# Optimization experiments

Measured on AMD Instinct MI355X. Metric: run time of the kernel, lower is better.

Reference implementation:

```python
import jax, jax.numpy as jnp
import numpy as np

EPS = 1e-12
ALPHA = 0.2  # LeakyReLU negative slope
N_NODES = 100000
N_EDGES = 1600000
F = 128
H = 8

def setup_inputs() -> dict:
    key = jax.random.key(0)
    k1, k2, k3, k4 = jax.random.split(key, 4)
    x = jax.random.normal(k1, (N_NODES, F), dtype=jnp.float32)
    row = jax.random.randint(k2, (N_EDGES,), 0, N_NODES, dtype=jnp.int32)
    col = jax.random.randint(k3, (N_EDGES,), 0, N_NODES, dtype=jnp.int32)
    # xavier_uniform with gain=1.414 on [H, 2F]
    limit = 1.414 * np.sqrt(6.0 / (H + 2 * F))
    aa = jax.random.uniform(k4, (H, 2 * F), dtype=jnp.float32, minval=-limit, maxval=limit)
    return {"x": x, "row": row, "col": col, "aa": aa}

def reference(x, row, col, aa):
    # e = leakyrelu(aa @ cat(x[row], x[col], dim=1).T)  -> [H, E]
    # Split aa so per-node scores are computed once, then gathered per edge
    # (identical math, avoids materializing the [E, 2F] concat).
    a_src, a_dst = aa[:, :F], aa[:, F:]          # [H, F] each
    s_src = x @ a_src.T                           # [N, H]
    s_dst = x @ a_dst.T                           # [N, H]
    e = s_src[row] + s_dst[col]                   # [E, H]
    e = jnp.where(e > 0, e, ALPHA * e)            # LeakyReLU
    # scatter_softmax over edges grouped by row (per head)
    m = jax.ops.segment_max(e, row, num_segments=N_NODES)  # [N, H]
    m = jnp.where(jnp.isfinite(m), m, 0.0)        # empty segments -> -inf; neutralize
    ex = jnp.exp(e - m[row])                      # [E, H]
    s = jax.ops.segment_sum(ex, row, num_segments=N_NODES)  # [N, H]
    a = ex / (s[row] + EPS)                       # [E, H]
    return a.T                                    # [H, E] to match torch layout
```

## Files before the change

kernel.cpp:

```cpp
#include <hip/hip_runtime.h>

constexpr int N_NODES = 100000;
constexpr int N_EDGES = 1600000;
constexpr int F = 128;
constexpr int H = 8;
constexpr float ALPHA = 0.2f;
constexpr float EPSF = 1e-12f;

constexpr int PSHIFT = 8;
constexpr int PN = 1 << PSHIFT;
constexpr int NPART = (N_NODES + PN - 1) / PN;
constexpr int MAXPART = 5120;
constexpr int EPB = 4096;
constexpr int OCAP = 4096;

constexpr int KA_BLOCKS = (N_EDGES + EPB - 1) / EPB;
constexpr int K1_BLOCKS = (N_NODES + 1023) / 1024;

static_assert(N_EDGES % 64 == 0, "k4_hs assumes 64-edge blocks");

__global__ void __launch_bounds__(1024)
kA1_fused(const int* __restrict__ row, const int* __restrict__ col,
          int* __restrict__ gcnt, unsigned* __restrict__ part,
          int* __restrict__ ocnt, int2* __restrict__ olist,
          const float* __restrict__ x, const float* __restrict__ aa,
          float* __restrict__ srn, float* __restrict__ sd) {
    __shared__ int hist[NPART];
    __shared__ int base[NPART];
    __shared__ float sa[H * 2 * F];
    const int t = threadIdx.x;

    if (blockIdx.x < KA_BLOCKS) {
        const int e0 = blockIdx.x * EPB;
        constexpr int K = EPB / 1024;
        int rr[K], cc[K];
        for (int p = t; p < NPART; p += 1024) hist[p] = 0;
        __syncthreads();
#pragma unroll
        for (int k = 0; k < K; ++k) {
            int i = e0 + k * 1024 + t;
            if (i < N_EDGES) {
                rr[k] = row[i];
                cc[k] = col[i];
                atomicAdd(&hist[rr[k] >> PSHIFT], 1);
            } else rr[k] = -1;
        }
        __syncthreads();
        for (int p = t; p < NPART; p += 1024) {
            int h = hist[p];
            base[p] = h ? atomicAdd(&gcnt[p], h) : 0;
            hist[p] = 0;
        }
        __syncthreads();
#pragma unroll
        for (int k = 0; k < K; ++k) {
            if (rr[k] >= 0) {
                int r = rr[k], c = cc[k];
                int p = r >> PSHIFT;
                int slot = base[p] + atomicAdd(&hist[p], 1);
                unsigned pk = ((unsigned)(r & (PN - 1)) << 17) | (unsigned)c;
                if (slot < MAXPART) {
                    part[(size_t)p * MAXPART + slot] = pk;
                } else {
                    int q = atomicAdd(ocnt, 1);
                    if (q < OCAP) olist[q] = make_int2(p, (int)pk);
                }
            }
        }
    } else {
        if (t < 512) reinterpret_cast<float4*>(sa)[t] =
            reinterpret_cast<const float4*>(aa)[t];
        __syncthreads();
        int node = (blockIdx.x - KA_BLOCKS) * 1024 + t;
        if (node >= N_NODES) return;
        const float4* xr = reinterpret_cast<const float4*>(x + (size_t)node * F);
        float accs[H], accd[H];
#pragma unroll
        for (int h = 0; h < H; ++h) { accs[h] = 0.f; accd[h] = 0.f; }
        for (int f4 = 0; f4 < F / 4; ++f4) {
            float4 xv = xr[f4];
#pragma unroll
            for (int h = 0; h < H; ++h) {
                float4 av = *reinterpret_cast<const float4*>(&sa[h * 2 * F + 4 * f4]);
                float4 bv = *reinterpret_cast<const float4*>(&sa[h * 2 * F + F + 4 * f4]);
                accs[h] += xv.x * av.x + xv.y * av.y + xv.z * av.z + xv.w * av.w;
                accd[h] += xv.x * bv.x + xv.y * bv.y + xv.z * bv.z + xv.w * bv.w;
            }
        }
        float4* os = reinterpret_cast<float4*>(srn + (size_t)node * 16);
        os[0] = make_float4(accs[0], accs[1], accs[2], accs[3]);
        os[1] = make_float4(accs[4], accs[5], accs[6], accs[7]);
        float4* od = reinterpret_cast<float4*>(sd + (size_t)node * H);
        od[0] = make_float4(accd[0], accd[1], accd[2], accd[3]);
        od[1] = make_float4(accd[4], accd[5], accd[6], accd[7]);
    }
}

__global__ void __launch_bounds__(1024)
kB_sum(const float* __restrict__ sd, const unsigned* __restrict__ part,
       const int* __restrict__ gcnt, const int* __restrict__ ocnt,
       const int2* __restrict__ olist, float* __restrict__ srn) {
    __shared__ unsigned plist[MAXPART];
    __shared__ unsigned sorted_c[MAXPART];
    __shared__ int hist[PN];
    __shared__ int off[PN + 1];
    __shared__ int cur[PN];
    __shared__ float ssrc[PN * H];
    const int p = blockIdx.x;
    const int t = threadIdx.x;
    const int nbase = p << PSHIFT;

    for (int i = t; i < PN; i += 1024) hist[i] = 0;
    for (int j = t; j < PN * H; j += 1024) {
        int n = nbase + (j >> 3);
        ssrc[j] = (n < N_NODES) ? srn[(size_t)n * 16 + (j & 7)] : 0.f;
    }
    __syncthreads();

    int cnt = gcnt[p]; if (cnt > MAXPART) cnt = MAXPART;
    const unsigned* pp = part + (size_t)p * MAXPART;

    for (int i = t; i < cnt; i += 1024) {
        unsigned pk = pp[i];
        plist[i] = pk;
        atomicAdd(&hist[pk >> 17], 1);
    }
    __syncthreads();

    if (t < 64) {
        int h0 = hist[4 * t], h1 = hist[4 * t + 1];
        int h2 = hist[4 * t + 2], h3 = hist[4 * t + 3];
        int s0 = h0, s1 = s0 + h1, s2 = s1 + h2, s3 = s2 + h3;
        int sc = s3;
#pragma unroll
        for (int d = 1; d < 64; d <<= 1) {
            int v = __shfl_up(sc, d);
            if (t >= d) sc += v;
        }
        int prefix = sc - s3;
        off[4 * t + 1] = prefix + s0; off[4 * t + 2] = prefix + s1;
        off[4 * t + 3] = prefix + s2; off[4 * t + 4] = prefix + s3;
        cur[4 * t]     = prefix;      cur[4 * t + 1] = prefix + s0;
        cur[4 * t + 2] = prefix + s1; cur[4 * t + 3] = prefix + s2;
        if (t == 0) off[0] = 0;
    }
    __syncthreads();

    for (int i = t; i < cnt; i += 1024) {
        unsigned pk = plist[i];
        int rl = (int)(pk >> 17);
        int slot = atomicAdd(&cur[rl], 1);
        sorted_c[slot] = pk & 0x1FFFFu;
    }
    __syncthreads();

    int mo = *ocnt; if (mo > OCAP) mo = OCAP;
    {
        int nl = t >> 2, pi = t & 3;
        int node = nbase + nl;
        int k0 = off[nl], k1e = off[nl + 1];
        float s0 = ssrc[nl * 8 + 2 * pi];
        float s1 = ssrc[nl * 8 + 2 * pi + 1];
        float a0 = 0.f, a1 = 0.f;
        int k = k0;
        for (; k + 4 <= k1e; k += 4) {
            int c0 = (int)sorted_c[k],     c1 = (int)sorted_c[k + 1];
            int c2 = (int)sorted_c[k + 2], c3 = (int)sorted_c[k + 3];
            float2 d0 = *reinterpret_cast<const float2*>(&sd[(size_t)c0 * H + 2 * pi]);
            float2 d1 = *reinterpret_cast<const float2*>(&sd[(size_t)c1 * H + 2 * pi]);
            float2 d2 = *reinterpret_cast<const float2*>(&sd[(size_t)c2 * H + 2 * pi]);
            float2 d3 = *reinterpret_cast<const float2*>(&sd[(size_t)c3 * H + 2 * pi]);
            float e;
            e = s0 + d0.x; e = e > 0.f ? e : ALPHA * e; a0 += __expf(e);
            e = s1 + d0.y; e = e > 0.f ? e : ALPHA * e; a1 += __expf(e);
            e = s0 + d1.x; e = e > 0.f ? e : ALPHA * e; a0 += __expf(e);
            e = s1 + d1.y; e = e > 0.f ? e : ALPHA * e; a1 += __expf(e);
            e = s0 + d2.x; e = e > 0.f ? e : ALPHA * e; a0 += __expf(e);
            e = s1 + d2.y; e = e > 0.f ? e : ALPHA * e; a1 += __expf(e);
            e = s0 + d3.x; e = e > 0.f ? e : ALPHA * e; a0 += __expf(e);
            e = s1 + d3.y; e = e > 0.f ? e : ALPHA * e; a1 += __expf(e);
        }
        for (; k < k1e; ++k) {
            int c = (int)sorted_c[k];
            float2 d = *reinterpret_cast<const float2*>(&sd[(size_t)c * H + 2 * pi]);
            float e0 = s0 + d.x; e0 = e0 > 0.f ? e0 : ALPHA * e0;
            float e1 = s1 + d.y; e1 = e1 > 0.f ? e1 : ALPHA * e1;
            a0 += __expf(e0); a1 += __expf(e1);
        }
        for (int j = 0; j < mo; ++j) {
            int2 oe = olist[j];
            if (oe.x == p && (int)(((unsigned)oe.y) >> 17) == nl) {
                int c = oe.y & 0x1FFFF;
                float2 d = *reinterpret_cast<const float2*>(&sd[(size_t)c * H + 2 * pi]);
                float e0 = s0 + d.x; e0 = e0 > 0.f ? e0 : ALPHA * e0;
                float e1 = s1 + d.y; e1 = e1 > 0.f ? e1 : ALPHA * e1;
                a0 += __expf(e0); a1 += __expf(e1);
            }
        }
        if (node < N_NODES) {
            srn[(size_t)node * 16 + 8 + 2 * pi]     = 1.f / (a0 + EPSF);
            srn[(size_t)node * 16 + 8 + 2 * pi + 1] = 1.f / (a1 + EPSF);
        }
    }
}

__global__ void __launch_bounds__(512)
k4_hs(const int* __restrict__ row, const int* __restrict__ col,
      const float* __restrict__ srn, const float* __restrict__ sd,
      float* __restrict__ out) {
    __shared__ int ridx[64], cidx[64];
    __shared__ float sm[8][72];
    const int e0 = blockIdx.x * 64;
    const int t = threadIdx.x;
    if (t < 64) ridx[t] = row[e0 + t];
    else if (t < 128) cidx[t - 64] = col[e0 + t - 64];
    __syncthreads();
    {
        int el = t >> 3, h = t & 7;
        int r = ridx[el], c = cidx[el];
        float s  = srn[(size_t)r * 16 + h];
        float rv = srn[(size_t)r * 16 + 8 + h];
        float d  = sd[(size_t)c * H + h];
        float e = s + d;
        e = e > 0.f ? e : ALPHA * e;
        sm[h][el] = __expf(e) * rv;
    }
    __syncthreads();
    {
        int h2 = t >> 6, j = t & 63;
        out[(size_t)h2 * N_EDGES + e0 + j] = sm[h2][j];
    }
}

__global__ void k1_scores(const float* __restrict__ x, const float* __restrict__ aa,
                          float* __restrict__ srn, float* __restrict__ sd) {
    __shared__ float sa[H * 2 * F];
    for (int i = threadIdx.x; i < H * 2 * F; i += blockDim.x) sa[i] = aa[i];
    __syncthreads();
    int node = blockIdx.x * blockDim.x + threadIdx.x;
    if (node >= N_NODES) return;
    const float4* xr = reinterpret_cast<const float4*>(x + (size_t)node * F);
    float accs[H], accd[H];
#pragma unroll
    for (int h = 0; h < H; ++h) { accs[h] = 0.f; accd[h] = 0.f; }
    for (int f4 = 0; f4 < F / 4; ++f4) {
        float4 xv = xr[f4];
#pragma unroll
        for (int h = 0; h < H; ++h) {
            float4 av = *reinterpret_cast<const float4*>(&sa[h * 2 * F + 4 * f4]);
            float4 bv = *reinterpret_cast<const float4*>(&sa[h * 2 * F + F + 4 * f4]);
            accs[h] += xv.x * av.x + xv.y * av.y + xv.z * av.z + xv.w * av.w;
            accd[h] += xv.x * bv.x + xv.y * bv.y + xv.z * bv.z + xv.w * bv.w;
        }
    }
    float4* os = reinterpret_cast<float4*>(srn + (size_t)node * 16);
    os[0] = make_float4(accs[0], accs[1], accs[2], accs[3]);
    os[1] = make_float4(accs[4], accs[5], accs[6], accs[7]);
    float4* od = reinterpret_cast<float4*>(sd + (size_t)node * H);
    od[0] = make_float4(accd[0], accd[1], accd[2], accd[3]);
    od[1] = make_float4(accd[4], accd[5], accd[6], accd[7]);
}

__global__ void kz_zero_sums(float* __restrict__ srn) {
    int t = blockIdx.x * blockDim.x + threadIdx.x;
    if (t >= N_NODES * H) return;
    srn[(size_t)(t >> 3) * 16 + 8 + (t & 7)] = 0.f;
}

__global__ void k3nm_sum(const float* __restrict__ srn_ro, const float* __restrict__ s_dst,
                         const int* __restrict__ row, const int* __restrict__ col,
                         float* __restrict__ srn) {
    int i = blockIdx.x * blockDim.x + threadIdx.x;
    if (i >= N_EDGES) return;
    int r = row[i], c = col[i];
    const float4* sr = reinterpret_cast<const float4*>(srn_ro + (size_t)r * 16);
    float4 a0 = sr[0], a1 = sr[1];
    const float4* sc = reinterpret_cast<const float4*>(s_dst + (size_t)c * H);
    float4 b0 = sc[0], b1 = sc[1];
    float ev[H] = {a0.x + b0.x, a0.y + b0.y, a0.z + b0.z, a0.w + b0.w,
                   a1.x + b1.x, a1.y + b1.y, a1.z + b1.z, a1.w + b1.w};
#pragma unroll
    for (int h = 0; h < H; ++h) {
        float e = ev[h] > 0.f ? ev[h] : ALPHA * ev[h];
        atomicAdd(&srn[(size_t)r * 16 + 8 + h], __expf(e));
    }
}

__global__ void k_inv(float* __restrict__ srn) {
    int t = blockIdx.x * blockDim.x + threadIdx.x;
    if (t >= N_NODES * H) return;
    int n = t >> 3, h = t & 7;
    float s = srn[(size_t)n * 16 + 8 + h];
    srn[(size_t)n * 16 + 8 + h] = 1.0f / (s + EPSF);
}

__global__ void k4_out(const int* __restrict__ row, const int* __restrict__ col,
                       const float* __restrict__ srn, const float* __restrict__ s_dst,
                       float* __restrict__ out) {
    int i = blockIdx.x * blockDim.x + threadIdx.x;
    if (i >= N_EDGES) return;
    int r = row[i], c = col[i];
    const float4* sr = reinterpret_cast<const float4*>(srn + (size_t)r * 16);
    float4 a0 = sr[0], a1 = sr[1], r0 = sr[2], r1 = sr[3];
    const float4* sc = reinterpret_cast<const float4*>(s_dst + (size_t)c * H);
    float4 b0 = sc[0], b1 = sc[1];
    float ev[H] = {a0.x + b0.x, a0.y + b0.y, a0.z + b0.z, a0.w + b0.w,
                   a1.x + b1.x, a1.y + b1.y, a1.z + b1.z, a1.w + b1.w};
    float rv[H] = {r0.x, r0.y, r0.z, r0.w, r1.x, r1.y, r1.z, r1.w};
#pragma unroll
    for (int h = 0; h < H; ++h) {
        float e = ev[h] > 0.f ? ev[h] : ALPHA * ev[h];
        out[(size_t)h * N_EDGES + i] = __expf(e) * rv[h];
    }
}

extern "C" void kernel_launch(void* const* d_in, const int* in_sizes, int n_in,
                              void* d_out, int out_size, void* d_ws, size_t ws_size,
                              hipStream_t stream) {
    const float* x   = (const float*)d_in[0];
    const int*   row = (const int*)d_in[1];
    const int*   col = (const int*)d_in[2];
    const float* aa  = (const float*)d_in[3];
    float* out = (float*)d_out;

    float*    srn  = (float*)d_ws;
    float*    sd   = srn + (size_t)N_NODES * 16;
    unsigned* part = (unsigned*)(sd + (size_t)N_NODES * H);
    int*      gcnt = (int*)(part + (size_t)NPART * MAXPART);
    int*      ocnt = gcnt + NPART;
    int2*     olist = (int2*)(ocnt + 16);

    const size_t need_b = ((size_t)N_NODES * 24 + (size_t)NPART * MAXPART
                           + NPART + 16 + 2 * OCAP) * 4;

    const int B = 256;
    const int GE = (N_EDGES + B - 1) / B;
    const int GN = (N_NODES + B - 1) / B;

    if (ws_size >= need_b) {
        hipMemsetAsync(gcnt, 0, (size_t)(NPART + 16) * sizeof(int), stream);
        kA1_fused<<<KA_BLOCKS + K1_BLOCKS, 1024, 0, stream>>>(
            row, col, gcnt, part, ocnt, olist, x, aa, srn, sd);
        kB_sum<<<NPART, 1024, 0, stream>>>(sd, part, gcnt, ocnt, olist, srn);
        k4_hs<<<N_EDGES / 64, 512, 0, stream>>>(row, col, srn, sd, out);
    } else {
        k1_scores<<<GN, B, 0, stream>>>(x, aa, srn, sd);
        kz_zero_sums<<<(N_NODES * H + B - 1) / B, B, 0, stream>>>(srn);
        k3nm_sum<<<GE, B, 0, stream>>>(srn, sd, row, col, srn);
        k_inv<<<(N_NODES * H + B - 1) / B, B, 0, stream>>>(srn);
        k4_out<<<GE, B, 0, stream>>>(row, col, srn, sd, out);
    }
}
```

Before: 211.2 us.

## Replace global-atomic partition bucketing with per-block fixed-capacity cells

The edge bucketing pass stops using global atomics and a memset. Each 256-thread block now writes its edges into fixed 24-slot cells per partition, plus a small per-block overflow list. The sum kernel gathers the cells for its partition from all producer blocks, building its histogram and counting sort straight from global memory. The score blocks also compute two nodes per thread with smaller blocks. In exchange, the cell array is sparse and strided to read, the sum kernel reads the part buffer twice, and overflow handling walks every block's overflow list.

```diff
diff --git a/kernel.cpp b/kernel.cpp
--- a/kernel.cpp
+++ b/kernel.cpp
@@ -10,120 +10,139 @@
 constexpr int PSHIFT = 8;
 constexpr int PN = 1 << PSHIFT;
 constexpr int NPART = (N_NODES + PN - 1) / PN;
-constexpr int MAXPART = 5120;
 constexpr int EPB = 4096;
-constexpr int OCAP = 4096;
-
 constexpr int KA_BLOCKS = (N_EDGES + EPB - 1) / EPB;
-constexpr int K1_BLOCKS = (N_NODES + 1023) / 1024;
+constexpr int CAP = 24;
+constexpr int OC2 = 32;
+constexpr int K1_NPB = 512;
+constexpr int K1_BLOCKS = (N_NODES + K1_NPB - 1) / K1_NPB;
+constexpr int NCELL = NPART * CAP;
 
 static_assert(N_EDGES % 64 == 0, "k4_hs assumes 64-edge blocks");
 
-__global__ void __launch_bounds__(1024)
+__global__ void __launch_bounds__(256)
 kA1_fused(const int* __restrict__ row, const int* __restrict__ col,
-          int* __restrict__ gcnt, unsigned* __restrict__ part,
-          int* __restrict__ ocnt, int2* __restrict__ olist,
+          unsigned* __restrict__ part2, int* __restrict__ cnt2,
+          int* __restrict__ ocnt2, int2* __restrict__ oflow2,
           const float* __restrict__ x, const float* __restrict__ aa,
           float* __restrict__ srn, float* __restrict__ sd) {
-    __shared__ int hist[NPART];
-    __shared__ int base[NPART];
-    __shared__ float sa[H * 2 * F];
     const int t = threadIdx.x;
-
     if (blockIdx.x < KA_BLOCKS) {
-        const int e0 = blockIdx.x * EPB;
-        constexpr int K = EPB / 1024;
-        int rr[K], cc[K];
-        for (int p = t; p < NPART; p += 1024) hist[p] = 0;
+        __shared__ int lcnt[NPART];
+        __shared__ int lof;
+        const int b = blockIdx.x;
+        const int e0 = b * EPB;
+        for (int p = t; p < NPART; p += 256) lcnt[p] = 0;
+        if (t == 0) lof = 0;
         __syncthreads();
 #pragma unroll
-        for (int k = 0; k < K; ++k) {
-            int i = e0 + k * 1024 + t;
+        for (int k = 0; k < EPB / 256; ++k) {
+            int i = e0 + k * 256 + t;
             if (i < N_EDGES) {
-                rr[k] = row[i];
-                cc[k] = col[i];
-                atomicAdd(&hist[rr[k] >> PSHIFT], 1);
-            } else rr[k] = -1;
-        }
-        __syncthreads();
-        for (int p = t; p < NPART; p += 1024) {
-            int h = hist[p];
-            base[p] = h ? atomicAdd(&gcnt[p], h) : 0;
-            hist[p] = 0;
-        }
-        __syncthreads();
-#pragma unroll
-        for (int k = 0; k < K; ++k) {
-            if (rr[k] >= 0) {
-                int r = rr[k], c = cc[k];
+                int r = row[i], c = col[i];
                 int p = r >> PSHIFT;
-                int slot = base[p] + atomicAdd(&hist[p], 1);
                 unsigned pk = ((unsigned)(r & (PN - 1)) << 17) | (unsigned)c;
-                if (slot < MAXPART) {
-                    part[(size_t)p * MAXPART + slot] = pk;
+                int slot = atomicAdd(&lcnt[p], 1);
+                if (slot < CAP) {
+                    part2[((size_t)p * KA_BLOCKS + b) * CAP + slot] = pk;
                 } else {
-                    int q = atomicAdd(ocnt, 1);
-                    if (q < OCAP) olist[q] = make_int2(p, (int)pk);
+                    int q = atomicAdd(&lof, 1);
+                    if (q < OC2) oflow2[b * OC2 + q] = make_int2(p, (int)pk);
                 }
             }
         }
+        __syncthreads();
+        for (int p = t; p < NPART; p += 256) {
+            int v = lcnt[p];
+            cnt2[(size_t)b * NPART + p] = v < CAP ? v : CAP;
+        }
+        if (t == 0) { int v = lof; ocnt2[b] = v < OC2 ? v : OC2; }
     } else {
-        if (t < 512) reinterpret_cast<float4*>(sa)[t] =
-            reinterpret_cast<const float4*>(aa)[t];
+        __shared__ float sa[H * 2 * F];
+        reinterpret_cast<float4*>(sa)[t]       = reinterpret_cast<const float4*>(aa)[t];
+        reinterpret_cast<float4*>(sa)[t + 256] = reinterpret_cast<const float4*>(aa)[t + 256];
         __syncthreads();
-        int node = (blockIdx.x - KA_BLOCKS) * 1024 + t;
-        if (node >= N_NODES) return;
-        const float4* xr = reinterpret_cast<const float4*>(x + (size_t)node * F);
-        float accs[H], accd[H];
-#pragma unroll
-        for (int h = 0; h < H; ++h) { accs[h] = 0.f; accd[h] = 0.f; }
+        const int q = blockIdx.x - KA_BLOCKS;
+        int n0 = q * K1_NPB + t;
+        int n1 = n0 + 256;
+        int n0c = n0 < N_NODES ? n0 : N_NODES - 1;
+        int n1c = n1 < N_NODES ? n1 : N_NODES - 1;
+        const float4* xr0 = reinterpret_cast<const float4*>(x + (size_t)n0c * F);
+        const float4* xr1 = reinterpret_cast<const float4*>(x + (size_t)n1c * F);
+        float a0s[H], a0d[H], a1s[H], a1d[H];
+#pragma unroll
+        for (int h = 0; h < H; ++h) { a0s[h] = 0.f; a0d[h] = 0.f; a1s[h] = 0.f; a1d[h] = 0.f; }
         for (int f4 = 0; f4 < F / 4; ++f4) {
-            float4 xv = xr[f4];
+            float4 xv0 = xr0[f4];
+            float4 xv1 = xr1[f4];
 #pragma unroll
             for (int h = 0; h < H; ++h) {
                 float4 av = *reinterpret_cast<const float4*>(&sa[h * 2 * F + 4 * f4]);
                 float4 bv = *reinterpret_cast<const float4*>(&sa[h * 2 * F + F + 4 * f4]);
-                accs[h] += xv.x * av.x + xv.y * av.y + xv.z * av.z + xv.w * av.w;
-                accd[h] += xv.x * bv.x + xv.y * bv.y + xv.z * bv.z + xv.w * bv.w;
+                a0s[h] += xv0.x * av.x + xv0.y * av.y + xv0.z * av.z + xv0.w * av.w;
+                a0d[h] += xv0.x * bv.x + xv0.y * bv.y + xv0.z * bv.z + xv0.w * bv.w;
+                a1s[h] += xv1.x * av.x + xv1.y * av.y + xv1.z * av.z + xv1.w * av.w;
+                a1d[h] += xv1.x * bv.x + xv1.y * bv.y + xv1.z * bv.z + xv1.w * bv.w;
             }
         }
-        float4* os = reinterpret_cast<float4*>(srn + (size_t)node * 16);
-        os[0] = make_float4(accs[0], accs[1], accs[2], accs[3]);
-        os[1] = make_float4(accs[4], accs[5], accs[6], accs[7]);
-        float4* od = reinterpret_cast<float4*>(sd + (size_t)node * H);
-        od[0] = make_float4(accd[0], accd[1], accd[2], accd[3]);
-        od[1] = make_float4(accd[4], accd[5], accd[6], accd[7]);
+        if (n0 < N_NODES) {
+            float4* os = reinterpret_cast<float4*>(srn + (size_t)n0 * 16);
+            os[0] = make_float4(a0s[0], a0s[1], a0s[2], a0s[3]);
+            os[1] = make_float4(a0s[4], a0s[5], a0s[6], a0s[7]);
+            float4* od = reinterpret_cast<float4*>(sd + (size_t)n0 * H);
+            od[0] = make_float4(a0d[0], a0d[1], a0d[2], a0d[3]);
+            od[1] = make_float4(a0d[4], a0d[5], a0d[6], a0d[7]);
+        }
+        if (n1 < N_NODES) {
+            float4* os = reinterpret_cast<float4*>(srn + (size_t)n1 * 16);
+            os[0] = make_float4(a1s[0], a1s[1], a1s[2], a1s[3]);
+            os[1] = make_float4(a1s[4], a1s[5], a1s[6], a1s[7]);
+            float4* od = reinterpret_cast<float4*>(sd + (size_t)n1 * H);
+            od[0] = make_float4(a1d[0], a1d[1], a1d[2], a1d[3]);
+            od[1] = make_float4(a1d[4], a1d[5], a1d[6], a1d[7]);
+        }
     }
 }
 
 __global__ void __launch_bounds__(1024)
-kB_sum(const float* __restrict__ sd, const unsigned* __restrict__ part,
-       const int* __restrict__ gcnt, const int* __restrict__ ocnt,
-       const int2* __restrict__ olist, float* __restrict__ srn) {
-    __shared__ unsigned plist[MAXPART];
-    __shared__ unsigned sorted_c[MAXPART];
+kB_sum(const float* __restrict__ sd, const unsigned* __restrict__ part2,
+       const int* __restrict__ cnt2, const int* __restrict__ ocnt2,
+       const int2* __restrict__ oflow2, float* __restrict__ srn) {
+    __shared__ unsigned sorted_c[NCELL];
     __shared__ int hist[PN];
     __shared__ int off[PN + 1];
     __shared__ int cur[PN];
     __shared__ float ssrc[PN * H];
+    __shared__ int lcb[NPART];
+    __shared__ int locnt[NPART];
+    __shared__ int otot;
     const int p = blockIdx.x;
     const int t = threadIdx.x;
     const int nbase = p << PSHIFT;
 
+    if (t == 0) otot = 0;
     for (int i = t; i < PN; i += 1024) hist[i] = 0;
     for (int j = t; j < PN * H; j += 1024) {
         int n = nbase + (j >> 3);
         ssrc[j] = (n < N_NODES) ? srn[(size_t)n * 16 + (j & 7)] : 0.f;
     }
-    __syncthreads();
-
-    int cnt = gcnt[p]; if (cnt > MAXPART) cnt = MAXPART;
-    const unsigned* pp = part + (size_t)p * MAXPART;
-
-    for (int i = t; i < cnt; i += 1024) {
-        unsigned pk = pp[i];
-        plist[i] = pk;
-        atomicAdd(&hist[pk >> 17], 1);
+    for (int b = t; b < NPART; b += 1024) {
+        lcb[b] = cnt2[(size_t)b * NPART + p];
+        int v = ocnt2[b];
+        locnt[b] = v;
+        if (v) atomicAdd(&otot, v);
+    }
+    __syncthreads();
+
+    const unsigned* pbase = part2 + (size_t)p * KA_BLOCKS * CAP;
+
+    for (int j = t; j < NCELL; j += 1024) {
+        int b = (int)(((unsigned)j * 21846u) >> 19);
+        int s = j - b * CAP;
+        if (s < lcb[b]) {
+            unsigned pk = pbase[(size_t)b * CAP + s];
+            atomicAdd(&hist[pk >> 17], 1);
+        }
     }
     __syncthreads();
 
@@ -146,15 +165,17 @@
     }
     __syncthreads();
 
-    for (int i = t; i < cnt; i += 1024) {
-        unsigned pk = plist[i];
-        int rl = (int)(pk >> 17);
-        int slot = atomicAdd(&cur[rl], 1);
-        sorted_c[slot] = pk & 0x1FFFFu;
-    }
-    __syncthreads();
-
-    int mo = *ocnt; if (mo > OCAP) mo = OCAP;
+    for (int j = t; j < NCELL; j += 1024) {
+        int b = (int)(((unsigned)j * 21846u) >> 19);
+        int s = j - b * CAP;
+        if (s < lcb[b]) {
+            unsigned pk = pbase[(size_t)b * CAP + s];
+            int slot = atomicAdd(&cur[pk >> 17], 1);
+            sorted_c[slot] = pk & 0x1FFFFu;
+        }
+    }
+    __syncthreads();
+
     {
         int nl = t >> 2, pi = t & 3;
         int node = nbase + nl;
@@ -187,14 +208,19 @@
             float e1 = s1 + d.y; e1 = e1 > 0.f ? e1 : ALPHA * e1;
             a0 += __expf(e0); a1 += __expf(e1);
         }
-        for (int j = 0; j < mo; ++j) {
-            int2 oe = olist[j];
-            if (oe.x == p && (int)(((unsigned)oe.y) >> 17) == nl) {
-                int c = oe.y & 0x1FFFF;
-                float2 d = *reinterpret_cast<const float2*>(&sd[(size_t)c * H + 2 * pi]);
-                float e0 = s0 + d.x; e0 = e0 > 0.f ? e0 : ALPHA * e0;
-                float e1 = s1 + d.y; e1 = e1 > 0.f ? e1 : ALPHA * e1;
-                a0 += __expf(e0); a1 += __expf(e1);
+        if (otot > 0) {
+            for (int b = 0; b < NPART; ++b) {
+                int m = locnt[b];
+                for (int j = 0; j < m; ++j) {
+                    int2 e2 = oflow2[b * OC2 + j];
+                    if (e2.x == p && (int)(((unsigned)e2.y) >> 17) == nl) {
+                        int c = e2.y & 0x1FFFF;
+                        float2 d = *reinterpret_cast<const float2*>(&sd[(size_t)c * H + 2 * pi]);
+                        float e0 = s0 + d.x; e0 = e0 > 0.f ? e0 : ALPHA * e0;
+                        float e1 = s1 + d.y; e1 = e1 > 0.f ? e1 : ALPHA * e1;
+                        a0 += __expf(e0); a1 += __expf(e1);
+                    }
+                }
             }
         }
         if (node < N_NODES) {
@@ -323,27 +349,30 @@
     const float* aa  = (const float*)d_in[3];
     float* out = (float*)d_out;
 
-    float*    srn  = (float*)d_ws;
-    float*    sd   = srn + (size_t)N_NODES * 16;
-    unsigned* part = (unsigned*)(sd + (size_t)N_NODES * H);
-    int*      gcnt = (int*)(part + (size_t)NPART * MAXPART);
-    int*      ocnt = gcnt + NPART;
-    int2*     olist = (int2*)(ocnt + 16);
-
-    const size_t need_b = ((size_t)N_NODES * 24 + (size_t)NPART * MAXPART
-                           + NPART + 16 + 2 * OCAP) * 4;
+    float*    srn   = (float*)d_ws;
+    float*    sd    = srn + (size_t)N_NODES * 16;
+    unsigned* part2 = (unsigned*)(sd + (size_t)N_NODES * H);
+    int*      cnt2  = (int*)(part2 + (size_t)NPART * KA_BLOCKS * CAP);
+    int*      ocnt2 = cnt2 + (size_t)KA_BLOCKS * NPART;
+    int2*     oflow2 = (int2*)(ocnt2 + KA_BLOCKS);
+
+    const size_t need_full = (size_t)(N_NODES * 24) * 4
+                           + (size_t)NPART * KA_BLOCKS * CAP * 4
+                           + (size_t)KA_BLOCKS * NPART * 4
+                           + (size_t)KA_BLOCKS * 4
+                           + (size_t)KA_BLOCKS * OC2 * 8;
+    const size_t need_min  = (size_t)N_NODES * (16 + 8) * 4;
 
     const int B = 256;
     const int GE = (N_EDGES + B - 1) / B;
     const int GN = (N_NODES + B - 1) / B;
 
-    if (ws_size >= need_b) {
-        hipMemsetAsync(gcnt, 0, (size_t)(NPART + 16) * sizeof(int), stream);
-        kA1_fused<<<KA_BLOCKS + K1_BLOCKS, 1024, 0, stream>>>(
-            row, col, gcnt, part, ocnt, olist, x, aa, srn, sd);
-        kB_sum<<<NPART, 1024, 0, stream>>>(sd, part, gcnt, ocnt, olist, srn);
+    if (ws_size >= need_full) {
+        kA1_fused<<<KA_BLOCKS + K1_BLOCKS, 256, 0, stream>>>(
+            row, col, part2, cnt2, ocnt2, oflow2, x, aa, srn, sd);
+        kB_sum<<<NPART, 1024, 0, stream>>>(sd, part2, cnt2, ocnt2, oflow2, srn);
         k4_hs<<<N_EDGES / 64, 512, 0, stream>>>(row, col, srn, sd, out);
-    } else {
+    } else if (ws_size >= need_min) {
         k1_scores<<<GN, B, 0, stream>>>(x, aa, srn, sd);
         kz_zero_sums<<<(N_NODES * H + B - 1) / B, B, 0, stream>>>(srn);
         k3nm_sum<<<GE, B, 0, stream>>>(srn, sd, row, col, srn);
```

Result: slower. 254.1 us (+20.3%).
